# Performance work log

Hardware: AMD Instinct MI355X
Metric: run time of the kernel (lower is better)

Reference implementation:

```python
import jax, jax.numpy as jnp
import numpy as np

B, T, E = 2, 1024, 1024
H, HD = 8, 128            # n_heads, head_dim
WS = 64                   # window_size (< T -> sliding-window branch)
TAU = 10.0
SCALE = 1.0 / np.sqrt(HD)


def setup_inputs() -> dict:
    key = jax.random.key(0)
    ks = jax.random.split(key, 8)
    s = 0.02
    return {
        "h": jax.random.normal(ks[0], (B, T, E), jnp.float32),
        "coord_1d": jax.random.uniform(ks[1], (B, T), jnp.float32),
        "Wq_w": jax.random.normal(ks[2], (E, E), jnp.float32) * s,
        "Wq_b": jnp.zeros((E,), jnp.float32),
        "Wk_w": jax.random.normal(ks[3], (E, E), jnp.float32) * s,
        "Wk_b": jnp.zeros((E,), jnp.float32),
        "Wv_w": jax.random.normal(ks[4], (E, E), jnp.float32) * s,
        "Wv_b": jnp.zeros((E,), jnp.float32),
        "Wo_w": jax.random.normal(ks[5], (E, E), jnp.float32) * s,
        "Wo_b": jnp.zeros((E,), jnp.float32),
    }


def reference(h, coord_1d, Wq_w, Wq_b, Wk_w, Wk_b, Wv_w, Wv_b, Wo_w, Wo_b):
    # sort positions by 1-D coordinate
    sort_idx = jnp.argsort(coord_1d, axis=1)          # (B,T)
    inv_idx = jnp.argsort(sort_idx, axis=1)
    h_s = jnp.take_along_axis(h, sort_idx[:, :, None], axis=1)  # (B,T,E)
    c_s = jnp.take_along_axis(coord_1d, sort_idx, axis=1)       # (B,T)

    def proj(w, b):
        return (h_s @ w.T + b).reshape(B, T, H, HD).transpose(0, 2, 1, 3)  # (B,H,T,HD)

    Q, K, V = proj(Wq_w, Wq_b), proj(Wk_w, Wk_b), proj(Wv_w, Wv_b)

    # centered sliding-window indices, clamped at sequence edges: (T, WS)
    pos = jnp.arange(T)
    start = jnp.clip(pos - WS // 2, 0, None)
    overflow = jnp.clip(start + WS - T, 0, None)
    start = jnp.clip(start - overflow, 0, None)
    base_idx = start[:, None] + jnp.arange(WS)

    # sorted-sequence position of depot (original index 0)
    depot = jnp.argmax(sort_idx == 0, axis=1)         # (B,)

    # append forced depot column -> (B,T,WS+1)
    idx_ext = jnp.concatenate(
        [jnp.broadcast_to(base_idx[None], (B, T, WS)),
         jnp.broadcast_to(depot[:, None, None], (B, T, 1))], axis=2)
    has_depot = jnp.any(base_idx[None] == depot[:, None, None], axis=2)  # (B,T)
    keep = jnp.concatenate(
        [jnp.ones((B, T, WS), bool), (~has_depot)[:, :, None]], axis=2)  # (B,T,WS+1)

    # gather windowed K/V: (B,H,T,WS+1,HD)
    gather_kv = jax.vmap(lambda x, idx: x[:, idx, :])
    K_w = gather_kv(K, idx_ext)
    V_w = gather_kv(V, idx_ext)

    scores = jnp.einsum('bhtd,bhtwd->bhtw', Q, K_w) * SCALE
    c_w = jax.vmap(lambda c, idx: c[idx])(c_s, idx_ext)          # (B,T,WS+1)
    dist2 = (c_w - c_s[:, :, None]) ** 2
    scores = scores - dist2[:, None] / TAU
    neg = jnp.finfo(scores.dtype).min
    scores = jnp.where(keep[:, None], scores, neg)
    attn = jax.nn.softmax(scores, axis=-1)
    ctx = jnp.einsum('bhtw,bhtwd->bhtd', attn, V_w)
    local_out = ctx.transpose(0, 2, 1, 3).reshape(B, T, E) @ Wo_w.T + Wo_b

    # depot attends to the full sequence
    Qd = jax.vmap(lambda q, d: q[:, d, :])(Q, depot)             # (B,H,HD)
    sd = jnp.einsum('bhd,bhtd->bht', Qd, K) * SCALE
    cd = jnp.take_along_axis(c_s, depot[:, None], axis=1)        # (B,1)
    sd = sd - ((c_s - cd) ** 2)[:, None] / TAU
    ad = jax.nn.softmax(sd, axis=-1)
    ctxd = jnp.einsum('bht,bhtd->bhd', ad, V).reshape(B, E) @ Wo_w.T + Wo_b

    out_sorted = local_out.at[jnp.arange(B), depot].set(ctxd)
    return jnp.take_along_axis(out_sorted, inv_idx[:, :, None], axis=1)
```

## Files before the change

kernel.cpp:

```cpp
#include <hip/hip_runtime.h>
#include <hip/hip_bf16.h>
#include <cmath>

constexpr int BB_ = 2;
constexpr int T_  = 1024;
constexpr int E_  = 1024;
constexpr int H_  = 8;
constexpr int HD_ = 128;
constexpr int WS_ = 64;
constexpr float TAU_   = 10.0f;
constexpr float SCALE_ = 0.08838834764831843f;

typedef __attribute__((ext_vector_type(8))) _Float16 half8;
typedef __attribute__((ext_vector_type(4))) _Float16 half4;
typedef __attribute__((ext_vector_type(4))) float floatx4;

constexpr int STB_ = 16;

__global__ __launch_bounds__(256) void sort_rank_kernel(
    const float* __restrict__ coord, int* __restrict__ sidx,
    float* __restrict__ c_s, int* __restrict__ depot) {
  __shared__ float c[T_];
  const int nb = T_ / STB_;
  const int b = blockIdx.x / nb;
  const int t0 = (blockIdx.x % nb) * STB_;
  const float* cb = coord + (size_t)b * T_;
  for (int i = threadIdx.x; i < T_; i += 256) c[i] = cb[i];
  __syncthreads();
  const int tl = threadIdx.x >> 4;
  const int ch = threadIdx.x & 15;
  const int t = t0 + tl;
  const float ct = c[t];
  int rank = 0;
  const int u0 = ch * (T_ / 16);
  #pragma unroll 8
  for (int i = 0; i < T_ / 16; ++i) {
    const int u = u0 + i;
    const float cu = c[u];
    rank += (cu < ct) || (cu == ct && u < t);
  }
  #pragma unroll
  for (int o = 8; o > 0; o >>= 1) rank += __shfl_xor(rank, o);
  if (ch == 0) {
    sidx[b * T_ + rank] = t;
    c_s[b * T_ + rank] = ct;
    if (t == 0) depot[b] = rank;
  }
}

__global__ __launch_bounds__(256) void convert_gather_h(
    const float* __restrict__ h, const int* __restrict__ sidx,
    _Float16* __restrict__ Ah) {
  const int gr = blockIdx.x;
  const int srow = (gr & ~(T_ - 1)) + sidx[gr];
  const float4 v = *(const float4*)(h + (size_t)srow * E_ + threadIdx.x * 4);
  half4 hv;
  hv.x = (_Float16)v.x; hv.y = (_Float16)v.y;
  hv.z = (_Float16)v.z; hv.w = (_Float16)v.w;
  *(half4*)(Ah + (size_t)gr * E_ + threadIdx.x * 4) = hv;
}

struct WConv {
  const float* src[4];
  _Float16* dst[4];
};

__global__ __launch_bounds__(256) void convert_w_kernel(WConv a) {
  const int z = blockIdx.z;
  const size_t idx = ((size_t)blockIdx.x * 256 + threadIdx.x) * 4;
  const float4 v = *(const float4*)(a.src[z] + idx);
  half4 hv;
  hv.x = (_Float16)v.x; hv.y = (_Float16)v.y;
  hv.z = (_Float16)v.z; hv.w = (_Float16)v.w;
  *(half4*)(a.dst[z] + idx) = hv;
}

struct GemmArgs {
  const _Float16* W[3];
  const float* bias[3];
  float* Cf[3];
  _Float16* Ch[3];
};

constexpr int LP_ = 56;

template <int BM, int BN, int SCATTER, int FP16OUT>
__global__ __launch_bounds__(256, 2) void gemm_f16(
    GemmArgs args, const _Float16* __restrict__ A,
    const int* __restrict__ sidx) {
  constexpr int TMI = BM / 32;
  constexpr int TNI = BN / 32;
  const _Float16* __restrict__ W = args.W[blockIdx.z];
  const float* __restrict__ bias = args.bias[blockIdx.z];

  __shared__ _Float16 As[BM][LP_], Bs[BN][LP_];

  const int tid = threadIdx.x;
  const int wv = tid >> 6, lane = tid & 63;
  const int kq = lane >> 4, ln15 = lane & 15;
  const int wm0 = (wv >> 1) * (BM / 2), wn0 = (wv & 1) * (BN / 2);
  const int m0 = blockIdx.y * BM, n0 = blockIdx.x * BN;

  floatx4 acc[TMI][TNI];
  #pragma unroll
  for (int i = 0; i < TMI; ++i)
    #pragma unroll
    for (int j = 0; j < TNI; ++j) acc[i][j] = (floatx4){0.f, 0.f, 0.f, 0.f};

  for (int k0 = 0; k0 < E_; k0 += 32) {
    #pragma unroll
    for (int i = 0; i < BM * 4 / 256; ++i) {
      const int idx = tid + 256 * i;
      const int r = idx >> 2, c = idx & 3;
      *(half8*)&As[r][c * 8] =
          *(const half8*)(A + (size_t)(m0 + r) * E_ + k0 + c * 8);
    }
    #pragma unroll
    for (int i = 0; i < BN * 4 / 256; ++i) {
      const int idx = tid + 256 * i;
      const int r = idx >> 2, c = idx & 3;
      *(half8*)&Bs[r][c * 8] =
          *(const half8*)(W + (size_t)(n0 + r) * E_ + k0 + c * 8);
    }
    __syncthreads();

    half8 ah[TMI], bf[TNI];
    #pragma unroll
    for (int mi = 0; mi < TMI; ++mi)
      ah[mi] = *(const half8*)&As[wm0 + mi * 16 + ln15][kq * 8];
    #pragma unroll
    for (int ni = 0; ni < TNI; ++ni)
      bf[ni] = *(const half8*)&Bs[wn0 + ni * 16 + ln15][kq * 8];
    #pragma unroll
    for (int mi = 0; mi < TMI; ++mi)
      #pragma unroll
      for (int ni = 0; ni < TNI; ++ni)
        acc[mi][ni] = __builtin_amdgcn_mfma_f32_16x16x32_f16(
            ah[mi], bf[ni], acc[mi][ni], 0, 0, 0);
    __syncthreads();
  }

  float* __restrict__ Cf = args.Cf[blockIdx.z];
  _Float16* __restrict__ Ch = args.Ch[blockIdx.z];
  #pragma unroll
  for (int ni = 0; ni < TNI; ++ni) {
    const int col = n0 + wn0 + ni * 16 + ln15;
    const float bv = bias[col];
    #pragma unroll
    for (int mi = 0; mi < TMI; ++mi) {
      #pragma unroll
      for (int r = 0; r < 4; ++r) {
        const int m = m0 + wm0 + mi * 16 + kq * 4 + r;
        const int orow = SCATTER ? ((m & ~(T_ - 1)) + sidx[m]) : m;
        const float val = acc[mi][ni][r] + bv;
        if (FP16OUT) {
          Ch[(size_t)orow * E_ + col] = (_Float16)val;
        } else {
          Cf[(size_t)orow * E_ + col] = val;
        }
      }
    }
  }
}

constexpr int QTm_ = 16;
constexpr int NSL_ = 80;

__global__ __launch_bounds__(256) void attn_local_kernel(
    const _Float16* __restrict__ Qh, const _Float16* __restrict__ Kh,
    const _Float16* __restrict__ Vh, const float* __restrict__ c_s,
    const int* __restrict__ depot, _Float16* __restrict__ CTh) {
  __shared__ float sc[QTm_][88];
  __shared__ float cw[NSL_];
  __shared__ float cq[QTm_];
  __shared__ float kdep[HD_];

  const int tid = threadIdx.x;
  const int ntq = T_ / QTm_;
  const int tq = blockIdx.x % ntq;
  const int bh = blockIdx.x / ntq;
  const int h = bh % H_, b = bh / H_;
  const int t0 = tq * QTm_;
  const int dep = depot[b];
  const int smin = min(max(t0 - 32, 0), T_ - WS_);
  const size_t baseBH = ((size_t)b * T_) * E_ + (size_t)h * HD_;

  if (tid < NSL_) {
    cw[tid] = c_s[b * T_ + min(smin + tid, T_ - 1)];
  } else if (tid < NSL_ + QTm_) {
    cq[tid - NSL_] = c_s[b * T_ + t0 + tid - NSL_];
  } else if (tid >= 128) {
    const int d = tid - 128;
    kdep[d] = (float)Kh[baseBH + (size_t)dep * E_ + d];
  }
  __syncthreads();

  const int wv = tid >> 6, lane = tid & 63;
  const int ln15 = lane & 15, kq = lane >> 4;

  {
    const size_t qoff = baseBH + (size_t)(t0 + ln15) * E_ + kq * 8;
    half8 aH[4];
    #pragma unroll
    for (int ks = 0; ks < 4; ++ks)
      aH[ks] = *(const half8*)(Qh + qoff + ks * 32);
    for (int kt = wv; kt < 5; kt += 4) {
      const int key = min(smin + kt * 16 + ln15, T_ - 1);
      const size_t koff = baseBH + (size_t)key * E_ + kq * 8;
      floatx4 acc = (floatx4){0.f, 0.f, 0.f, 0.f};
      #pragma unroll
      for (int ks = 0; ks < 4; ++ks) {
        const half8 b8 = *(const half8*)(Kh + koff + ks * 32);
        acc = __builtin_amdgcn_mfma_f32_16x16x32_f16(aH[ks], b8, acc, 0, 0, 0);
      }
      #pragma unroll
      for (int r = 0; r < 4; ++r)
        sc[kq * 4 + r][kt * 16 + ln15] = acc[r];
    }
  }

  const float cdep = c_s[b * T_ + dep];
  #pragma unroll
  for (int qi = 0; qi < 4; ++qi) {
    const int q = wv * 4 + qi;
    const int t = t0 + q;
    const size_t qo2 = baseBH + (size_t)t * E_;
    const float q1 = (float)Qh[qo2 + lane];
    const float q2 = (float)Qh[qo2 + 64 + lane];
    float part = fmaf(q1, kdep[lane], q2 * kdep[lane + 64]);
    #pragma unroll
    for (int o = 32; o > 0; o >>= 1) part += __shfl_xor(part, o);
    if (lane == 0) {
      const int st = min(max(t - 32, 0), T_ - WS_);
      const bool masked = (unsigned)(dep - st) < (unsigned)WS_;
      const float dd = cdep - cq[q];
      sc[q][80] = masked ? -3.0e38f
                         : part * SCALE_ - dd * dd * (1.0f / TAU_);
    }
  }
  __syncthreads();

  #pragma unroll
  for (int qi = 0; qi < 4; ++qi) {
    const int q = wv * 4 + qi;
    const int t = t0 + q;
    const int st = min(max(t - 32, 0), T_ - WS_);
    const int base = st - smin;
    const float cqv = cq[q];
    const int j1 = lane;
    float s1 = -3.0e38f;
    if (j1 >= base && j1 < base + WS_) {
      const float dd = cw[j1] - cqv;
      s1 = sc[q][j1] * SCALE_ - dd * dd * (1.0f / TAU_);
    }
    const int j2 = 64 + lane;
    float s2 = -3.0e38f;
    if (lane < 16 && j2 >= base && j2 < base + WS_) {
      const float dd = cw[j2] - cqv;
      s2 = sc[q][j2] * SCALE_ - dd * dd * (1.0f / TAU_);
    }
    const float sdep = sc[q][80];
    float m = fmaxf(s1, s2);
    #pragma unroll
    for (int o = 32; o > 0; o >>= 1) m = fmaxf(m, __shfl_xor(m, o));
    m = fmaxf(m, sdep);
    const float e1 = expf(s1 - m);
    const float e2 = (lane < 16) ? expf(s2 - m) : 0.f;
    float sum = e1 + e2;
    #pragma unroll
    for (int o = 32; o > 0; o >>= 1) sum += __shfl_xor(sum, o);
    const float edep = expf(sdep - m);
    sum += edep;
    const float inv = 1.0f / sum;
    sc[q][j1] = e1 * inv;
    if (lane < 16) sc[q][j2] = e2 * inv;
    if (lane == 0) sc[q][80] = edep * inv;
  }
  __syncthreads();

  {
    const int d1 = lane, d2 = lane + 64;
    float acc0[4], acc1[4];
    #pragma unroll
    for (int qi = 0; qi < 4; ++qi) { acc0[qi] = 0.f; acc1[qi] = 0.f; }
    for (int j = 0; j <= NSL_; ++j) {
      const int row = (j < NSL_) ? min(smin + j, T_ - 1) : dep;
      const size_t vo = baseBH + (size_t)row * E_;
      const float v1 = (float)Vh[vo + d1];
      const float v2 = (float)Vh[vo + d2];
      #pragma unroll
      for (int qi = 0; qi < 4; ++qi) {
        const float w = sc[wv * 4 + qi][j];
        acc0[qi] = fmaf(w, v1, acc0[qi]);
        acc1[qi] = fmaf(w, v2, acc1[qi]);
      }
    }
    #pragma unroll
    for (int qi = 0; qi < 4; ++qi) {
      const int t = t0 + wv * 4 + qi;
      const size_t co = baseBH + (size_t)t * E_;
      CTh[co + d1] = (_Float16)acc0[qi];
      CTh[co + d2] = (_Float16)acc1[qi];
    }
  }
}

constexpr int DCH_ = 16;
constexpr int VSP_ = 8;

__global__ __launch_bounds__(256) void depot_scores_kernel(
    const _Float16* __restrict__ Qh, const _Float16* __restrict__ Kh,
    const float* __restrict__ c_s, const int* __restrict__ depot,
    float* __restrict__ scg) {
  const int chunk = blockIdx.x % DCH_;
  const int bh = blockIdx.x / DCH_;
  const int h = bh % H_, b = bh / H_;
  const int tid = threadIdx.x, wv = tid >> 6, lane = tid & 63;
  const int dep = depot[b];
  const size_t baseBH = ((size_t)b * T_) * E_ + (size_t)h * HD_;
  __shared__ float qd[HD_];
  if (tid < HD_) qd[tid] = (float)Qh[baseBH + (size_t)dep * E_ + tid];
  __syncthreads();
  const float cdep = c_s[b * T_ + dep];
  constexpr int KPB = T_ / DCH_;
  const int k0 = chunk * KPB + wv * (KPB / 4);
  #pragma unroll 4
  for (int i = 0; i < KPB / 4; ++i) {
    const int k = k0 + i;
    const size_t ko = baseBH + (size_t)k * E_;
    const float k1 = (float)Kh[ko + lane];
    const float k2 = (float)Kh[ko + 64 + lane];
    float part = fmaf(qd[lane], k1, qd[lane + 64] * k2);
    #pragma unroll
    for (int o = 32; o > 0; o >>= 1) part += __shfl_xor(part, o);
    if (lane == 0) {
      const float dd = c_s[b * T_ + k] - cdep;
      scg[bh * T_ + k] = part * SCALE_ - dd * dd * (1.0f / TAU_);
    }
  }
}

__global__ __launch_bounds__(256) void depot_softmax_kernel(
    float* __restrict__ scg) {
  __shared__ float sc[T_];
  __shared__ float red[4];
  const int bh = blockIdx.x;
  const int tid = threadIdx.x, wv = tid >> 6, lane = tid & 63;
  float* s = scg + bh * T_;
  float lm = -3.0e38f;
  for (int k = tid; k < T_; k += 256) { sc[k] = s[k]; lm = fmaxf(lm, sc[k]); }
  #pragma unroll
  for (int o = 32; o > 0; o >>= 1) lm = fmaxf(lm, __shfl_xor(lm, o));
  if (lane == 0) red[wv] = lm;
  __syncthreads();
  const float M = fmaxf(fmaxf(red[0], red[1]), fmaxf(red[2], red[3]));
  __syncthreads();
  float ls = 0.f;
  float ev[T_ / 256];
  #pragma unroll
  for (int i = 0; i < T_ / 256; ++i) {
    ev[i] = expf(sc[tid + 256 * i] - M);
    ls += ev[i];
  }
  #pragma unroll
  for (int o = 32; o > 0; o >>= 1) ls += __shfl_xor(ls, o);
  if (lane == 0) red[wv] = ls;
  __syncthreads();
  const float inv = 1.0f / (red[0] + red[1] + red[2] + red[3]);
  #pragma unroll
  for (int i = 0; i < T_ / 256; ++i) s[tid + 256 * i] = ev[i] * inv;
}

__global__ __launch_bounds__(256) void depot_ctx_kernel(
    const _Float16* __restrict__ Vh, const float* __restrict__ scg,
    float* __restrict__ part) {
  __shared__ float par[2][HD_];
  const int sp = blockIdx.x % VSP_;
  const int bh = blockIdx.x / VSP_;
  const int h = bh % H_, b = bh / H_;
  const int tid = threadIdx.x;
  const int d = tid & 127, kg = tid >> 7;
  const size_t baseBH = ((size_t)b * T_) * E_ + (size_t)h * HD_;
  constexpr int KPB = T_ / VSP_;
  const int k0 = sp * KPB + kg * (KPB / 2);
  const _Float16* vbase = Vh + baseBH + d;
  const float* a = scg + bh * T_;
  float acc = 0.f;
  #pragma unroll 8
  for (int k = k0; k < k0 + KPB / 2; ++k) {
    acc = fmaf(a[k], (float)vbase[(size_t)k * E_], acc);
  }
  par[kg][d] = acc;
  __syncthreads();
  if (tid < HD_) part[((size_t)sp * BB_ * H_ + bh) * HD_ + tid] =
      par[0][tid] + par[1][tid];
}

__global__ __launch_bounds__(256) void depot_write_kernel(
    const float* __restrict__ part, const int* __restrict__ depot,
    _Float16* __restrict__ CTh) {
  for (int o = threadIdx.x; o < BB_ * H_ * HD_; o += 256) {
    const int bh = o >> 7, d = o & 127;
    float s = 0.f;
    #pragma unroll
    for (int sp = 0; sp < VSP_; ++sp)
      s += part[((size_t)sp * BB_ * H_ + bh) * HD_ + d];
    const int h = bh % H_, b = bh / H_;
    const int dep = depot[b];
    CTh[((size_t)b * T_ + dep) * E_ + (size_t)h * HD_ + d] = (_Float16)s;
  }
}

extern "C" void kernel_launch(void* const* d_in, const int* in_sizes, int n_in,
                              void* d_out, int out_size, void* d_ws, size_t ws_size,
                              hipStream_t stream) {
  const float* h     = (const float*)d_in[0];
  const float* coord = (const float*)d_in[1];
  const float* Wq    = (const float*)d_in[2];
  const float* Wqb   = (const float*)d_in[3];
  const float* Wk    = (const float*)d_in[4];
  const float* Wkb   = (const float*)d_in[5];
  const float* Wv    = (const float*)d_in[6];
  const float* Wvb   = (const float*)d_in[7];
  const float* Wo    = (const float*)d_in[8];
  const float* Wob   = (const float*)d_in[9];
  float* out = (float*)d_out;

  char* ws = (char*)d_ws;
  const size_t MATH_ = (size_t)BB_ * T_ * E_ * 2;
  const size_t WB   = (size_t)E_ * E_ * 2;
  size_t off = 0;
  _Float16* Qh  = (_Float16*)(ws + off); off += MATH_;
  _Float16* Kh  = (_Float16*)(ws + off); off += MATH_;
  _Float16* Vh  = (_Float16*)(ws + off); off += MATH_;
  _Float16* Ah  = (_Float16*)(ws + off); off += MATH_;
  _Float16* CTh = (_Float16*)(ws + off); off += MATH_;
  _Float16* Wh[4];
  for (int i = 0; i < 4; ++i) { Wh[i] = (_Float16*)(ws + off); off += WB; }
  float* c_s = (float*)(ws + off); off += (size_t)BB_ * T_ * 4;
  int* sidx  = (int*)(ws + off);   off += (size_t)BB_ * T_ * 4;
  int* depo  = (int*)(ws + off);   off += 256;
  float* scg  = (float*)(ws + off); off += (size_t)BB_ * H_ * T_ * 4;
  float* dpar = (float*)(ws + off); off += (size_t)VSP_ * BB_ * H_ * HD_ * 4;

  sort_rank_kernel<<<BB_ * (T_ / STB_), 256, 0, stream>>>(coord, sidx, c_s, depo);

  convert_gather_h<<<BB_ * T_, 256, 0, stream>>>(h, sidx, Ah);

  WConv wc;
  wc.src[0] = Wq; wc.src[1] = Wk; wc.src[2] = Wv; wc.src[3] = Wo;
  for (int i = 0; i < 4; ++i) wc.dst[i] = Wh[i];
  convert_w_kernel<<<dim3(E_ * E_ / 1024, 1, 4), 256, 0, stream>>>(wc);

  GemmArgs qa;
  qa.W[0] = Wh[0]; qa.W[1] = Wh[1]; qa.W[2] = Wh[2];
  qa.bias[0] = Wqb; qa.bias[1] = Wkb; qa.bias[2] = Wvb;
  qa.Cf[0] = qa.Cf[1] = qa.Cf[2] = nullptr;
  qa.Ch[0] = Qh; qa.Ch[1] = Kh; qa.Ch[2] = Vh;
  gemm_f16<128, 64, 0, 1><<<dim3(E_ / 64, (BB_ * T_) / 128, 3), 256, 0, stream>>>(
      qa, Ah, sidx);

  attn_local_kernel<<<BB_ * H_ * (T_ / QTm_), 256, 0, stream>>>(
      Qh, Kh, Vh, c_s, depo, CTh);

  depot_scores_kernel<<<BB_ * H_ * DCH_, 256, 0, stream>>>(
      Qh, Kh, c_s, depo, scg);
  depot_softmax_kernel<<<BB_ * H_, 256, 0, stream>>>(scg);
  depot_ctx_kernel<<<BB_ * H_ * VSP_, 256, 0, stream>>>(Vh, scg, dpar);
  depot_write_kernel<<<1, 256, 0, stream>>>(dpar, depo, CTh);

  GemmArgs oa;
  oa.W[0] = oa.W[1] = oa.W[2] = Wh[3];
  oa.bias[0] = oa.bias[1] = oa.bias[2] = Wob;
  oa.Cf[0] = oa.Cf[1] = oa.Cf[2] = out;
  oa.Ch[0] = oa.Ch[1] = oa.Ch[2] = nullptr;
  gemm_f16<64, 64, 1, 0><<<dim3(E_ / 64, (BB_ * T_) / 64, 1), 256, 0, stream>>>(
      oa, CTh, sidx);
}
```

Before: 181.2 us.

## Fuse h gather/convert into QKV GEMM and depot scoring into local attention

Removes the separate convert_gather_h kernel: the QKV GEMM now loads fp32 rows of h through the sort index and converts them to fp16 while filling shared memory. Depot score computation moves into the local attention kernel, where each block scores its own 16 keys against the depot query, and the depot softmax is folded into depot_ctx_kernel. V loads and context stores are vectorized to half2. This drops launches and an intermediate fp16 buffer round-trip, at the cost of the GEMM reading twice as many bytes of A per tile and each ctx block redoing the softmax.

After: 169.4 us. -6.5%, faster.

```diff
diff --git a/kernel.cpp b/kernel.cpp
--- a/kernel.cpp
+++ b/kernel.cpp
@@ -13,6 +13,7 @@
 
 typedef __attribute__((ext_vector_type(8))) _Float16 half8;
 typedef __attribute__((ext_vector_type(4))) _Float16 half4;
+typedef __attribute__((ext_vector_type(2))) _Float16 half2v;
 typedef __attribute__((ext_vector_type(4))) float floatx4;
 
 constexpr int STB_ = 16;
@@ -48,18 +49,6 @@
   }
 }
 
-__global__ __launch_bounds__(256) void convert_gather_h(
-    const float* __restrict__ h, const int* __restrict__ sidx,
-    _Float16* __restrict__ Ah) {
-  const int gr = blockIdx.x;
-  const int srow = (gr & ~(T_ - 1)) + sidx[gr];
-  const float4 v = *(const float4*)(h + (size_t)srow * E_ + threadIdx.x * 4);
-  half4 hv;
-  hv.x = (_Float16)v.x; hv.y = (_Float16)v.y;
-  hv.z = (_Float16)v.z; hv.w = (_Float16)v.w;
-  *(half4*)(Ah + (size_t)gr * E_ + threadIdx.x * 4) = hv;
-}
-
 struct WConv {
   const float* src[4];
   _Float16* dst[4];
@@ -84,16 +73,16 @@
 
 constexpr int LP_ = 56;
 
-template <int BM, int BN, int SCATTER, int FP16OUT>
+template <int BM, int BN, int GATHER, int SCATTER, int FP16OUT>
 __global__ __launch_bounds__(256, 2) void gemm_f16(
-    GemmArgs args, const _Float16* __restrict__ A,
-    const int* __restrict__ sidx) {
+    GemmArgs args, const void* __restrict__ Av, const int* __restrict__ sidx) {
   constexpr int TMI = BM / 32;
   constexpr int TNI = BN / 32;
   const _Float16* __restrict__ W = args.W[blockIdx.z];
   const float* __restrict__ bias = args.bias[blockIdx.z];
 
   __shared__ _Float16 As[BM][LP_], Bs[BN][LP_];
+  __shared__ int srow[BM];
 
   const int tid = threadIdx.x;
   const int wv = tid >> 6, lane = tid & 63;
@@ -101,6 +90,14 @@
   const int wm0 = (wv >> 1) * (BM / 2), wn0 = (wv & 1) * (BN / 2);
   const int m0 = blockIdx.y * BM, n0 = blockIdx.x * BN;
 
+  if (GATHER) {
+    if (tid < BM) {
+      const int gr = m0 + tid;
+      srow[tid] = (gr & ~(T_ - 1)) + sidx[gr];
+    }
+    __syncthreads();
+  }
+
   floatx4 acc[TMI][TNI];
   #pragma unroll
   for (int i = 0; i < TMI; ++i)
@@ -108,12 +105,28 @@
     for (int j = 0; j < TNI; ++j) acc[i][j] = (floatx4){0.f, 0.f, 0.f, 0.f};
 
   for (int k0 = 0; k0 < E_; k0 += 32) {
-    #pragma unroll
-    for (int i = 0; i < BM * 4 / 256; ++i) {
-      const int idx = tid + 256 * i;
-      const int r = idx >> 2, c = idx & 3;
-      *(half8*)&As[r][c * 8] =
-          *(const half8*)(A + (size_t)(m0 + r) * E_ + k0 + c * 8);
+    if (GATHER) {
+      const float* A = (const float*)Av;
+      #pragma unroll
+      for (int i = 0; i < BM * 8 / 256; ++i) {
+        const int idx = tid + 256 * i;
+        const int r = idx >> 3, c4 = idx & 7;
+        const float4 v =
+            *(const float4*)(A + (size_t)srow[r] * E_ + k0 + c4 * 4);
+        half4 hv;
+        hv.x = (_Float16)v.x; hv.y = (_Float16)v.y;
+        hv.z = (_Float16)v.z; hv.w = (_Float16)v.w;
+        *(half4*)&As[r][c4 * 4] = hv;
+      }
+    } else {
+      const _Float16* A = (const _Float16*)Av;
+      #pragma unroll
+      for (int i = 0; i < BM * 4 / 256; ++i) {
+        const int idx = tid + 256 * i;
+        const int r = idx >> 2, c = idx & 3;
+        *(half8*)&As[r][c * 8] =
+            *(const half8*)(A + (size_t)(m0 + r) * E_ + k0 + c * 8);
+      }
     }
     #pragma unroll
     for (int i = 0; i < BN * 4 / 256; ++i) {
@@ -165,15 +178,18 @@
 
 constexpr int QTm_ = 16;
 constexpr int NSL_ = 80;
+constexpr int VSP_ = 8;
 
 __global__ __launch_bounds__(256) void attn_local_kernel(
     const _Float16* __restrict__ Qh, const _Float16* __restrict__ Kh,
     const _Float16* __restrict__ Vh, const float* __restrict__ c_s,
-    const int* __restrict__ depot, _Float16* __restrict__ CTh) {
+    const int* __restrict__ depot, _Float16* __restrict__ CTh,
+    float* __restrict__ scg) {
   __shared__ float sc[QTm_][88];
   __shared__ float cw[NSL_];
   __shared__ float cq[QTm_];
   __shared__ float kdep[HD_];
+  __shared__ float qdep[HD_];
 
   const int tid = threadIdx.x;
   const int ntq = T_ / QTm_;
@@ -193,6 +209,7 @@
     const int d = tid - 128;
     kdep[d] = (float)Kh[baseBH + (size_t)dep * E_ + d];
   }
+  if (tid < HD_) qdep[tid] = (float)Qh[baseBH + (size_t)dep * E_ + tid];
   __syncthreads();
 
   const int wv = tid >> 6, lane = tid & 63;
@@ -220,6 +237,7 @@
   }
 
   const float cdep = c_s[b * T_ + dep];
+
   #pragma unroll
   for (int qi = 0; qi < 4; ++qi) {
     const int q = wv * 4 + qi;
@@ -236,6 +254,21 @@
       const float dd = cdep - cq[q];
       sc[q][80] = masked ? -3.0e38f
                          : part * SCALE_ - dd * dd * (1.0f / TAU_);
+    }
+  }
+
+  #pragma unroll
+  for (int qi = 0; qi < 4; ++qi) {
+    const int k = t0 + wv * 4 + qi;
+    const size_t ko = baseBH + (size_t)k * E_;
+    const float k1 = (float)Kh[ko + lane];
+    const float k2 = (float)Kh[ko + 64 + lane];
+    float part = fmaf(qdep[lane], k1, qdep[lane + 64] * k2);
+    #pragma unroll
+    for (int o = 32; o > 0; o >>= 1) part += __shfl_xor(part, o);
+    if (lane == 0) {
+      const float dd = cw[k - smin] - cdep;
+      scg[bh * T_ + k] = part * SCALE_ - dd * dd * (1.0f / TAU_);
     }
   }
   __syncthreads();
@@ -279,15 +312,15 @@
   __syncthreads();
 
   {
-    const int d1 = lane, d2 = lane + 64;
+    const int dp = lane * 2;
     float acc0[4], acc1[4];
     #pragma unroll
     for (int qi = 0; qi < 4; ++qi) { acc0[qi] = 0.f; acc1[qi] = 0.f; }
     for (int j = 0; j <= NSL_; ++j) {
       const int row = (j < NSL_) ? min(smin + j, T_ - 1) : dep;
-      const size_t vo = baseBH + (size_t)row * E_;
-      const float v1 = (float)Vh[vo + d1];
-      const float v2 = (float)Vh[vo + d2];
+      const half2v v = *(const half2v*)(Vh + baseBH + (size_t)row * E_ + dp);
+      const float v1 = (float)v.x;
+      const float v2 = (float)v.y;
       #pragma unroll
       for (int qi = 0; qi < 4; ++qi) {
         const float w = sc[wv * 4 + qi][j];
@@ -298,97 +331,59 @@
     #pragma unroll
     for (int qi = 0; qi < 4; ++qi) {
       const int t = t0 + wv * 4 + qi;
-      const size_t co = baseBH + (size_t)t * E_;
-      CTh[co + d1] = (_Float16)acc0[qi];
-      CTh[co + d2] = (_Float16)acc1[qi];
-    }
-  }
-}
-
-constexpr int DCH_ = 16;
-constexpr int VSP_ = 8;
-
-__global__ __launch_bounds__(256) void depot_scores_kernel(
-    const _Float16* __restrict__ Qh, const _Float16* __restrict__ Kh,
-    const float* __restrict__ c_s, const int* __restrict__ depot,
-    float* __restrict__ scg) {
-  const int chunk = blockIdx.x % DCH_;
-  const int bh = blockIdx.x / DCH_;
-  const int h = bh % H_, b = bh / H_;
-  const int tid = threadIdx.x, wv = tid >> 6, lane = tid & 63;
-  const int dep = depot[b];
-  const size_t baseBH = ((size_t)b * T_) * E_ + (size_t)h * HD_;
-  __shared__ float qd[HD_];
-  if (tid < HD_) qd[tid] = (float)Qh[baseBH + (size_t)dep * E_ + tid];
-  __syncthreads();
-  const float cdep = c_s[b * T_ + dep];
-  constexpr int KPB = T_ / DCH_;
-  const int k0 = chunk * KPB + wv * (KPB / 4);
-  #pragma unroll 4
-  for (int i = 0; i < KPB / 4; ++i) {
-    const int k = k0 + i;
-    const size_t ko = baseBH + (size_t)k * E_;
-    const float k1 = (float)Kh[ko + lane];
-    const float k2 = (float)Kh[ko + 64 + lane];
-    float part = fmaf(qd[lane], k1, qd[lane + 64] * k2);
-    #pragma unroll
-    for (int o = 32; o > 0; o >>= 1) part += __shfl_xor(part, o);
-    if (lane == 0) {
-      const float dd = c_s[b * T_ + k] - cdep;
-      scg[bh * T_ + k] = part * SCALE_ - dd * dd * (1.0f / TAU_);
-    }
-  }
-}
-
-__global__ __launch_bounds__(256) void depot_softmax_kernel(
-    float* __restrict__ scg) {
-  __shared__ float sc[T_];
-  __shared__ float red[4];
-  const int bh = blockIdx.x;
-  const int tid = threadIdx.x, wv = tid >> 6, lane = tid & 63;
-  float* s = scg + bh * T_;
-  float lm = -3.0e38f;
-  for (int k = tid; k < T_; k += 256) { sc[k] = s[k]; lm = fmaxf(lm, sc[k]); }
-  #pragma unroll
-  for (int o = 32; o > 0; o >>= 1) lm = fmaxf(lm, __shfl_xor(lm, o));
-  if (lane == 0) red[wv] = lm;
-  __syncthreads();
-  const float M = fmaxf(fmaxf(red[0], red[1]), fmaxf(red[2], red[3]));
-  __syncthreads();
-  float ls = 0.f;
-  float ev[T_ / 256];
-  #pragma unroll
-  for (int i = 0; i < T_ / 256; ++i) {
-    ev[i] = expf(sc[tid + 256 * i] - M);
-    ls += ev[i];
-  }
-  #pragma unroll
-  for (int o = 32; o > 0; o >>= 1) ls += __shfl_xor(ls, o);
-  if (lane == 0) red[wv] = ls;
-  __syncthreads();
-  const float inv = 1.0f / (red[0] + red[1] + red[2] + red[3]);
-  #pragma unroll
-  for (int i = 0; i < T_ / 256; ++i) s[tid + 256 * i] = ev[i] * inv;
+      half2v o;
+      o.x = (_Float16)acc0[qi];
+      o.y = (_Float16)acc1[qi];
+      *(half2v*)(CTh + baseBH + (size_t)t * E_ + dp) = o;
+    }
+  }
 }
 
 __global__ __launch_bounds__(256) void depot_ctx_kernel(
     const _Float16* __restrict__ Vh, const float* __restrict__ scg,
     float* __restrict__ part) {
+  __shared__ float sc[T_];
+  __shared__ float red[4];
   __shared__ float par[2][HD_];
   const int sp = blockIdx.x % VSP_;
   const int bh = blockIdx.x / VSP_;
   const int h = bh % H_, b = bh / H_;
-  const int tid = threadIdx.x;
+  const int tid = threadIdx.x, wv = tid >> 6, lane = tid & 63;
+  const float* s = scg + bh * T_;
+
+  float lm = -3.0e38f;
+  for (int k = tid; k < T_; k += 256) { sc[k] = s[k]; lm = fmaxf(lm, sc[k]); }
+  #pragma unroll
+  for (int o = 32; o > 0; o >>= 1) lm = fmaxf(lm, __shfl_xor(lm, o));
+  if (lane == 0) red[wv] = lm;
+  __syncthreads();
+  const float M = fmaxf(fmaxf(red[0], red[1]), fmaxf(red[2], red[3]));
+  __syncthreads();
+  float ls = 0.f;
+  float ev[T_ / 256];
+  #pragma unroll
+  for (int i = 0; i < T_ / 256; ++i) {
+    ev[i] = expf(sc[tid + 256 * i] - M);
+    ls += ev[i];
+  }
+  #pragma unroll
+  for (int o = 32; o > 0; o >>= 1) ls += __shfl_xor(ls, o);
+  if (lane == 0) red[wv] = ls;
+  __syncthreads();
+  const float inv = 1.0f / (red[0] + red[1] + red[2] + red[3]);
+  #pragma unroll
+  for (int i = 0; i < T_ / 256; ++i) sc[tid + 256 * i] = ev[i] * inv;
+  __syncthreads();
+
   const int d = tid & 127, kg = tid >> 7;
   const size_t baseBH = ((size_t)b * T_) * E_ + (size_t)h * HD_;
   constexpr int KPB = T_ / VSP_;
   const int k0 = sp * KPB + kg * (KPB / 2);
   const _Float16* vbase = Vh + baseBH + d;
-  const float* a = scg + bh * T_;
   float acc = 0.f;
   #pragma unroll 8
   for (int k = k0; k < k0 + KPB / 2; ++k) {
-    acc = fmaf(a[k], (float)vbase[(size_t)k * E_], acc);
+    acc = fmaf(sc[k], (float)vbase[(size_t)k * E_], acc);
   }
   par[kg][d] = acc;
   __syncthreads();
@@ -433,7 +428,6 @@
   _Float16* Qh  = (_Float16*)(ws + off); off += MATH_;
   _Float16* Kh  = (_Float16*)(ws + off); off += MATH_;
   _Float16* Vh  = (_Float16*)(ws + off); off += MATH_;
-  _Float16* Ah  = (_Float16*)(ws + off); off += MATH_;
   _Float16* CTh = (_Float16*)(ws + off); off += MATH_;
   _Float16* Wh[4];
   for (int i = 0; i < 4; ++i) { Wh[i] = (_Float16*)(ws + off); off += WB; }
@@ -445,8 +439,6 @@
 
   sort_rank_kernel<<<BB_ * (T_ / STB_), 256, 0, stream>>>(coord, sidx, c_s, depo);
 
-  convert_gather_h<<<BB_ * T_, 256, 0, stream>>>(h, sidx, Ah);
-
   WConv wc;
   wc.src[0] = Wq; wc.src[1] = Wk; wc.src[2] = Wv; wc.src[3] = Wo;
   for (int i = 0; i < 4; ++i) wc.dst[i] = Wh[i];
@@ -457,15 +449,12 @@
   qa.bias[0] = Wqb; qa.bias[1] = Wkb; qa.bias[2] = Wvb;
   qa.Cf[0] = qa.Cf[1] = qa.Cf[2] = nullptr;
   qa.Ch[0] = Qh; qa.Ch[1] = Kh; qa.Ch[2] = Vh;
-  gemm_f16<128, 64, 0, 1><<<dim3(E_ / 64, (BB_ * T_) / 128, 3), 256, 0, stream>>>(
-      qa, Ah, sidx);
+  gemm_f16<128, 64, 1, 0, 1><<<dim3(E_ / 64, (BB_ * T_) / 128, 3), 256, 0, stream>>>(
+      qa, h, sidx);
 
   attn_local_kernel<<<BB_ * H_ * (T_ / QTm_), 256, 0, stream>>>(
-      Qh, Kh, Vh, c_s, depo, CTh);
-
-  depot_scores_kernel<<<BB_ * H_ * DCH_, 256, 0, stream>>>(
-      Qh, Kh, c_s, depo, scg);
-  depot_softmax_kernel<<<BB_ * H_, 256, 0, stream>>>(scg);
+      Qh, Kh, Vh, c_s, depo, CTh, scg);
+
   depot_ctx_kernel<<<BB_ * H_ * VSP_, 256, 0, stream>>>(Vh, scg, dpar);
   depot_write_kernel<<<1, 256, 0, stream>>>(dpar, depo, CTh);
 
@@ -474,6 +463,6 @@
   oa.bias[0] = oa.bias[1] = oa.bias[2] = Wob;
   oa.Cf[0] = oa.Cf[1] = oa.Cf[2] = out;
   oa.Ch[0] = oa.Ch[1] = oa.Ch[2] = nullptr;
-  gemm_f16<64, 64, 1, 0><<<dim3(E_ / 64, (BB_ * T_) / 64, 1), 256, 0, stream>>>(
+  gemm_f16<64, 64, 0, 1, 0><<<dim3(E_ / 64, (BB_ * T_) / 64, 1), 256, 0, stream>>>(
       oa, CTh, sidx);
 }
```
